# Kernel optimization log

Hardware: AMD Instinct MI355X
Metric: run time of the kernel (lower is better)

## Reference

```python
import jax, jax.numpy as jnp
import numpy as np

B, C, F, D = 128, 16, 128, 512


def setup_inputs() -> dict:
    key = jax.random.key(0)
    k1, k2 = jax.random.split(key)
    return {
        "c_feats": jax.random.normal(k1, (B, C, D), dtype=jnp.float32),
        "f_feats": jax.random.normal(k2, (B, F, D), dtype=jnp.float32),
    }


def _dtw_path_masks(S):
    """S: [P, c, f] per-pair similarity. Returns [P, c, f] 0/1 max-path masks.

    DP: D[i,j] = max(D[i-1,j], D[i,j-1], D[i-1,j-1]) + S[i-1,j-1], D[0,0]=0,
    borders -inf. Tie-break priority (up, left, diag) matches Python max().
    Row recurrence is vectorized: D[i,j] = Csum[j] + cummax_k<=j(A[k]-Csum[k-1])
    where A[k]=max(D[i-1,k], D[i-1,k-1]) (wavefront-free row-parallel form).
    """
    P_, c, f = S.shape
    NEG = -jnp.inf

    init = jnp.concatenate([jnp.zeros((P_, 1), S.dtype),
                            jnp.full((P_, f), NEG, S.dtype)], axis=1)  # D[0, 0..f]

    def row_step(prev, dt_row):
        # prev: [P, f+1] = D[i-1, 0..f]; dt_row: [P, f] = S[i-1, :]
        A = jnp.maximum(prev[:, 1:], prev[:, :-1])                  # max(D[i-1,j], D[i-1,j-1])
        Ccum = jnp.cumsum(dt_row, axis=1)
        Cm1 = jnp.concatenate([jnp.zeros((P_, 1), dt_row.dtype), Ccum[:, :-1]], axis=1)
        row = Ccum + jax.lax.cummax(A - Cm1, axis=1)                # D[i, 1..f]
        new_prev = jnp.concatenate([jnp.full((P_, 1), NEG, dt_row.dtype), row], axis=1)
        return new_prev, new_prev

    _, rows = jax.lax.scan(row_step, init, jnp.moveaxis(S, 1, 0))   # [c, P, f+1]
    Dm = jnp.moveaxis(jnp.concatenate([init[None], rows], axis=0), 1, 0)  # [P, c+1, f+1]

    # Predecessor choice per cell; argmax picks first max -> priority up,left,diag
    up = Dm[:, :-1, 1:]
    left = Dm[:, 1:, :-1]
    diag = Dm[:, :-1, :-1]
    mv = jnp.argmax(jnp.stack([up, left, diag], axis=-1), axis=-1).astype(jnp.int32)
    mv = jnp.pad(mv, ((0, 0), (1, 0), (1, 0)))                      # [P, c+1, f+1]

    pidx = jnp.arange(P_)

    def bt_step(carry, _):
        mask, i, j = carry
        active = (i > 0) | (j > 0)
        mask = mask.at[pidx, i - 1, j - 1].add(jnp.where(active, 1.0, 0.0).astype(mask.dtype))
        m = mv[pidx, i, j]
        di = jnp.where(m == 1, 0, 1)   # left keeps i
        dj = jnp.where(m == 0, 0, 1)   # up keeps j
        i = jnp.where(active, i - di, i)
        j = jnp.where(active, j - dj, j)
        return (mask, i, j), None

    mask0 = jnp.zeros((P_, c, f), jnp.float32)
    i0 = jnp.full((P_,), c, jnp.int32)
    j0 = jnp.full((P_,), f, jnp.int32)
    (mask, _, _), _ = jax.lax.scan(bt_step, (mask0, i0, j0), None, length=c + f)
    return mask


def reference(c_feats, f_feats):
    b, c, d = c_feats.shape
    f = f_feats.shape[1]
    xn = c_feats / jnp.linalg.norm(c_feats, axis=-1, keepdims=True)
    yn = f_feats / jnp.linalg.norm(f_feats, axis=-1, keepdims=True)
    # Source quirk: y row j is normalized only once outer index i reaches it
    # (y[i-1] bug), so S[i,j] uses normalized y[j] iff j <= i, raw y[j] otherwise.
    Sn = jnp.einsum('mcd,nfd->mncf', xn, yn)
    Sr = jnp.einsum('mcd,nfd->mncf', xn, f_feats)
    tri = jnp.arange(f)[None, :] <= jnp.arange(c)[:, None]          # [c, f]: j <= i
    S = jnp.where(tri, Sn, Sr).reshape(b * b, c, f)
    return _dtw_path_masks(S).reshape(b, b, c, f)
```

## Files before the change

### kernel.cpp

```cpp
#include <hip/hip_runtime.h>
#include <stdint.h>

#define M_TOT 2048
#define N_TOT 16384
#define K_TOT 512

typedef _Float16 f16x8 __attribute__((ext_vector_type(8)));
typedef float f32x4 __attribute__((ext_vector_type(4)));

#define AS1 __attribute__((address_space(1)))
#define AS3 __attribute__((address_space(3)))

__device__ __forceinline__ void ld_lds16(const void* g, void* l) {
    __builtin_amdgcn_global_load_lds((const AS1 void*)g, (AS3 void*)l, 16, 0, 0);
}

__device__ __forceinline__ void split4(float x0, float x1, float x2, float x3,
                                       uint2* hs, uint2* ls) {
    union U { _Float16 h[4]; uint2 u; } H, L;
    _Float16 h0 = (_Float16)x0; H.h[0] = h0; L.h[0] = (_Float16)(x0 - (float)h0);
    _Float16 h1 = (_Float16)x1; H.h[1] = h1; L.h[1] = (_Float16)(x1 - (float)h1);
    _Float16 h2 = (_Float16)x2; H.h[2] = h2; L.h[2] = (_Float16)(x2 - (float)h2);
    _Float16 h3 = (_Float16)x3; H.h[3] = h3; L.h[3] = (_Float16)(x3 - (float)h3);
    *hs = H.u; *ls = L.u;
}

__global__ __launch_bounds__(256) void norm_split_kernel(
    const float* __restrict__ c_feats, const float* __restrict__ f_feats,
    _Float16* __restrict__ Ah, _Float16* __restrict__ Al,
    _Float16* __restrict__ Bh, _Float16* __restrict__ Bl,
    float* __restrict__ normf)
{
    int wave = blockIdx.x * 4 + (threadIdx.x >> 6);
    int lane = threadIdx.x & 63;
    if (wave < 2048) {
        const float* row = c_feats + (size_t)wave * K_TOT;
        float4 v0 = ((const float4*)row)[lane];
        float4 v1 = ((const float4*)row)[lane + 64];
        double ss = (double)v0.x * v0.x + (double)v0.y * v0.y +
                    (double)v0.z * v0.z + (double)v0.w * v0.w +
                    (double)v1.x * v1.x + (double)v1.y * v1.y +
                    (double)v1.z * v1.z + (double)v1.w * v1.w;
        #pragma unroll
        for (int off = 32; off; off >>= 1) ss += __shfl_down(ss, off);
        double tot = __shfl(ss, 0);
        float nrm = sqrtf((float)tot);
        float a0 = v0.x / nrm, a1 = v0.y / nrm, a2 = v0.z / nrm, a3 = v0.w / nrm;
        float b0 = v1.x / nrm, b1 = v1.y / nrm, b2 = v1.z / nrm, b3 = v1.w / nrm;
        uint2 h, l;
        split4(a0, a1, a2, a3, &h, &l);
        ((uint2*)(Ah + (size_t)wave * K_TOT))[lane] = h;
        ((uint2*)(Al + (size_t)wave * K_TOT))[lane] = l;
        split4(b0, b1, b2, b3, &h, &l);
        ((uint2*)(Ah + (size_t)wave * K_TOT))[lane + 64] = h;
        ((uint2*)(Al + (size_t)wave * K_TOT))[lane + 64] = l;
    } else if (wave < 18432) {
        int fr = wave - 2048;
        const float* row = f_feats + (size_t)fr * K_TOT;
        float4 v0 = ((const float4*)row)[lane];
        float4 v1 = ((const float4*)row)[lane + 64];
        double ss = (double)v0.x * v0.x + (double)v0.y * v0.y +
                    (double)v0.z * v0.z + (double)v0.w * v0.w +
                    (double)v1.x * v1.x + (double)v1.y * v1.y +
                    (double)v1.z * v1.z + (double)v1.w * v1.w;
        #pragma unroll
        for (int off = 32; off; off >>= 1) ss += __shfl_down(ss, off);
        if (lane == 0) normf[fr] = sqrtf((float)ss);
        uint2 h, l;
        split4(v0.x, v0.y, v0.z, v0.w, &h, &l);
        ((uint2*)(Bh + (size_t)fr * K_TOT))[lane] = h;
        ((uint2*)(Bl + (size_t)fr * K_TOT))[lane] = l;
        split4(v1.x, v1.y, v1.z, v1.w, &h, &l);
        ((uint2*)(Bh + (size_t)fr * K_TOT))[lane + 64] = h;
        ((uint2*)(Bl + (size_t)fr * K_TOT))[lane + 64] = l;
    }
}

__global__ __launch_bounds__(256, 2) void mfma_gemm_kernel(
    const _Float16* __restrict__ Ah, const _Float16* __restrict__ Al,
    const _Float16* __restrict__ Bh, const _Float16* __restrict__ Bl,
    const float* __restrict__ normf,
    float* __restrict__ out)
{
    __shared__ _Float16 sAh[128 * 32];
    __shared__ _Float16 sAl[128 * 32];
    __shared__ _Float16 sBh[128 * 32];
    __shared__ _Float16 sBl[128 * 32];

    const int t = threadIdx.x;
    const int w = t >> 6, lane = t & 63;
    const int gm0 = blockIdx.y * 128, gn0 = blockIdx.x * 128;
    const int wm = (w & 1) * 64, wn = (w >> 1) * 64;
    const int fr = lane & 15, fq = lane >> 4;

    f32x4 acc[4][4] = {};

    const int l0 = w * 128 + lane;

    for (int k0 = 0; k0 < K_TOT; k0 += 32) {
        #pragma unroll
        for (int c = 0; c < 2; ++c) {
            int l = l0 + c * 64;
            int row = l >> 2, kq = l & 3;
            size_t goffA = (size_t)(gm0 + row) * K_TOT + k0 + kq * 8;
            size_t goffB = (size_t)(gn0 + row) * K_TOT + k0 + kq * 8;
            ld_lds16(Ah + goffA, sAh + (size_t)l * 8);
            ld_lds16(Al + goffA, sAl + (size_t)l * 8);
            ld_lds16(Bh + goffB, sBh + (size_t)l * 8);
            ld_lds16(Bl + goffB, sBl + (size_t)l * 8);
        }
        __syncthreads();

        f16x8 fah[4], fal[4], fbh[4], fbl[4];
        #pragma unroll
        for (int x = 0; x < 4; ++x) {
            int ar = (wm + x * 16 + fr) * 32 + fq * 8;
            int br = (wn + x * 16 + fr) * 32 + fq * 8;
            fah[x] = *(const f16x8*)(sAh + ar);
            fal[x] = *(const f16x8*)(sAl + ar);
            fbh[x] = *(const f16x8*)(sBh + br);
            fbl[x] = *(const f16x8*)(sBl + br);
        }
        #pragma unroll
        for (int mi = 0; mi < 4; ++mi)
            #pragma unroll
            for (int ni = 0; ni < 4; ++ni) {
                acc[mi][ni] = __builtin_amdgcn_mfma_f32_16x16x32_f16(fah[mi], fbl[ni], acc[mi][ni], 0, 0, 0);
                acc[mi][ni] = __builtin_amdgcn_mfma_f32_16x16x32_f16(fal[mi], fbh[ni], acc[mi][ni], 0, 0, 0);
                acc[mi][ni] = __builtin_amdgcn_mfma_f32_16x16x32_f16(fah[mi], fbh[ni], acc[mi][ni], 0, 0, 0);
            }
        __syncthreads();
    }

    const int nn = blockIdx.x;
    #pragma unroll
    for (int ni = 0; ni < 4; ++ni) {
        int col = wn + ni * 16 + fr;
        bool cn = (col < 16);
        float nf = 1.f;
        if (cn) nf = normf[gn0 + col];
        #pragma unroll
        for (int mi = 0; mi < 4; ++mi) {
            #pragma unroll
            for (int r = 0; r < 4; ++r) {
                int gm = gm0 + wm + mi * 16 + fq * 4 + r;
                int mm = gm >> 4, ii = gm & 15;
                float v = acc[mi][ni][r];
                if (cn && col <= ii) v /= nf;
                out[(((size_t)mm * 128 + nn) * 16 + ii) * 128 + col] = v;
            }
        }
    }
}

__global__ __launch_bounds__(256) void dtw_kernel(float* __restrict__ buf)
{
    const int lane = threadIdx.x & 63;
    const int p = blockIdx.x * 4 + (threadIdx.x >> 6);
    float* tile = buf + (size_t)p * 2048;
    const double NEG = -1e300;
    double pA = NEG, pB = NEG;
    unsigned mvA = 0, mvB = 0;

    for (int i = 1; i <= 16; ++i) {
        float2 s = ((const float2*)tile)[(i - 1) * 64 + lane];
        double s1 = (double)s.x;
        double s2 = s1 + (double)s.y;
        double t = s2;
        #pragma unroll
        for (int off = 1; off < 64; off <<= 1) {
            double u = __shfl_up(t, off);
            if (lane >= off) t += u;
        }
        double excl = t - s2;
        double C1 = excl + s1;
        double C2 = excl + s2;
        double pm1 = __shfl_up(pB, 1);
        if (lane == 0) pm1 = (i == 1) ? 0.0 : NEG;
        double A1 = fmax(pm1, pA);
        double A2 = fmax(pA, pB);
        double T1 = A1 - excl;
        double T2 = A2 - C1;
        double g = fmax(T1, T2);
        #pragma unroll
        for (int off = 1; off < 64; off <<= 1) {
            double u = __shfl_up(g, off);
            if (lane >= off) g = fmax(g, u);
        }
        double gex = __shfl_up(g, 1);
        if (lane == 0) gex = NEG;
        double M1 = fmax(gex, T1);
        double M2 = fmax(M1, T2);
        double nA = C1 + M1;
        double nB = C2 + M2;
        double lA = __shfl_up(nB, 1);
        if (lane == 0) lA = NEG;
        int m1 = (pA >= lA && pA >= pm1) ? 0 : ((lA >= pm1) ? 1 : 2);
        int m2v = (pB >= nA && pB >= pA) ? 0 : ((nA >= pA) ? 1 : 2);
        mvA |= (unsigned)m1 << (2 * (i - 1));
        mvB |= (unsigned)m2v << (2 * (i - 1));
        pA = nA; pB = nB;
    }

    unsigned maskA = 0, maskB = 0;
    int i = 16, j = 128;
    for (int step = 0; step < 160; ++step) {
        if (i <= 0 && j <= 0) break;
        int col = j - 1, row = i - 1;
        if (row < 0) { j -= 1; continue; }
        if (col < 0) { i -= 1; continue; }
        int owner = col >> 1, sub = col & 1;
        if (lane == owner) {
            if (sub) maskB |= 1u << row; else maskA |= 1u << row;
        }
        unsigned wmv = __shfl(sub ? mvB : mvA, owner);
        int m = (int)((wmv >> (2 * row)) & 3u);
        i -= (m == 1) ? 0 : 1;
        j -= (m == 0) ? 0 : 1;
    }

    #pragma unroll
    for (int r = 0; r < 16; ++r) {
        float2 v;
        v.x = (float)((maskA >> r) & 1u);
        v.y = (float)((maskB >> r) & 1u);
        ((float2*)tile)[r * 64 + lane] = v;
    }
}

extern "C" void kernel_launch(void* const* d_in, const int* in_sizes, int n_in,
                              void* d_out, int out_size, void* d_ws, size_t ws_size,
                              hipStream_t stream)
{
    const float* c_feats = (const float*)d_in[0];
    const float* f_feats = (const float*)d_in[1];
    float* out = (float*)d_out;

    _Float16* Ah = (_Float16*)d_ws;
    _Float16* Al = Ah + (size_t)M_TOT * K_TOT;
    _Float16* Bh = Al + (size_t)M_TOT * K_TOT;
    _Float16* Bl = Bh + (size_t)N_TOT * K_TOT;
    float* normf = (float*)(Bl + (size_t)N_TOT * K_TOT);

    norm_split_kernel<<<4608, 256, 0, stream>>>(c_feats, f_feats, Ah, Al, Bh, Bl, normf);
    dim3 g(N_TOT / 128, M_TOT / 128);
    mfma_gemm_kernel<<<g, 256, 0, stream>>>(Ah, Al, Bh, Bl, normf, out);
    dtw_kernel<<<16384 / 4, 256, 0, stream>>>(out);
}
```

Measured before the change: 386.5 us.

## Rewrite DTW as anti-diagonal wavefront with 16 lanes per pair and LDS backtrack

The DTW kernel changes from a row-parallel scan, with 64 lanes per pair and log-step shuffle scans for the cumsum and cummax, to an anti-diagonal wavefront. Each pair now gets 16 lanes, one per row, so each wave handles 4 pairs. Move codes go to LDS, and one lane per pair backtracks, recording each row's column range. All lanes then write the masks as coalesced float4 stores. This removes the log-depth shuffle scans, but adds a 143-step serial wavefront, a serial backtrack on one lane, and extra LDS use.

```diff
diff --git a/kernel.cpp b/kernel.cpp
--- a/kernel.cpp
+++ b/kernel.cpp
@@ -155,76 +155,81 @@
 
 __global__ __launch_bounds__(256) void dtw_kernel(float* __restrict__ buf)
 {
+    __shared__ uint8_t mv_lds[4][4][2064];
+    __shared__ int bounds[4][4][16];
+
     const int lane = threadIdx.x & 63;
-    const int p = blockIdx.x * 4 + (threadIdx.x >> 6);
+    const int w = threadIdx.x >> 6;
+    const int q = lane >> 4, r = lane & 15;
+    const int pbase = blockIdx.x * 16 + w * 4;
+    const int p = pbase + q;
     float* tile = buf + (size_t)p * 2048;
+    const float4* row4 = (const float4*)(tile + r * 128);
+    uint8_t* mymv = &mv_lds[w][q][0];
+
     const double NEG = -1e300;
-    double pA = NEG, pB = NEG;
-    unsigned mvA = 0, mvB = 0;
-
-    for (int i = 1; i <= 16; ++i) {
-        float2 s = ((const float2*)tile)[(i - 1) * 64 + lane];
-        double s1 = (double)s.x;
-        double s2 = s1 + (double)s.y;
-        double t = s2;
-        #pragma unroll
-        for (int off = 1; off < 64; off <<= 1) {
-            double u = __shfl_up(t, off);
-            if (lane >= off) t += u;
-        }
-        double excl = t - s2;
-        double C1 = excl + s1;
-        double C2 = excl + s2;
-        double pm1 = __shfl_up(pB, 1);
-        if (lane == 0) pm1 = (i == 1) ? 0.0 : NEG;
-        double A1 = fmax(pm1, pA);
-        double A2 = fmax(pA, pB);
-        double T1 = A1 - excl;
-        double T2 = A2 - C1;
-        double g = fmax(T1, T2);
-        #pragma unroll
-        for (int off = 1; off < 64; off <<= 1) {
-            double u = __shfl_up(g, off);
-            if (lane >= off) g = fmax(g, u);
-        }
-        double gex = __shfl_up(g, 1);
-        if (lane == 0) gex = NEG;
-        double M1 = fmax(gex, T1);
-        double M2 = fmax(M1, T2);
-        double nA = C1 + M1;
-        double nB = C2 + M2;
-        double lA = __shfl_up(nB, 1);
-        if (lane == 0) lA = NEG;
-        int m1 = (pA >= lA && pA >= pm1) ? 0 : ((lA >= pm1) ? 1 : 2);
-        int m2v = (pB >= nA && pB >= pA) ? 0 : ((nA >= pA) ? 1 : 2);
-        mvA |= (unsigned)m1 << (2 * (i - 1));
-        mvB |= (unsigned)m2v << (2 * (i - 1));
-        pA = nA; pB = nB;
-    }
-
-    unsigned maskA = 0, maskB = 0;
-    int i = 16, j = 128;
-    for (int step = 0; step < 160; ++step) {
-        if (i <= 0 && j <= 0) break;
-        int col = j - 1, row = i - 1;
-        if (row < 0) { j -= 1; continue; }
-        if (col < 0) { i -= 1; continue; }
-        int owner = col >> 1, sub = col & 1;
-        if (lane == owner) {
-            if (sub) maskB |= 1u << row; else maskA |= 1u << row;
-        }
-        unsigned wmv = __shfl(sub ? mvB : mvA, owner);
-        int m = (int)((wmv >> (2 * row)) & 3u);
-        i -= (m == 1) ? 0 : 1;
-        j -= (m == 0) ? 0 : 1;
-    }
-
-    #pragma unroll
-    for (int r = 0; r < 16; ++r) {
-        float2 v;
-        v.x = (float)((maskA >> r) & 1u);
-        v.y = (float)((maskB >> r) & 1u);
-        ((float2*)tile)[r * 64 + lane] = v;
+    double Dp = NEG, Dp2 = NEG;
+    float4 cur4 = {0, 0, 0, 0};
+    float4 nxt4 = row4[0];
+
+    for (int t = 0; t < 143; ++t) {
+        int j = t - r;
+        bool act = (j >= 0) & (j < 128);
+        if (act & ((j & 3) == 0)) {
+            cur4 = nxt4;
+            if (j + 4 < 128) nxt4 = row4[(j >> 2) + 1];
+        }
+        int e = j & 3;
+        float sv = (e == 0) ? cur4.x : (e == 1) ? cur4.y : (e == 2) ? cur4.z : cur4.w;
+        double up = __shfl_up(Dp, 1);
+        double dg = __shfl_up(Dp2, 1);
+        double lf = Dp;
+        if (r == 0) up = NEG;
+        if (j == 0) {
+            lf = NEG;
+            dg = (r == 0) ? 0.0 : NEG;
+        } else if (r == 0) {
+            dg = NEG;
+        }
+        int m = (up >= lf && up >= dg) ? 0 : ((lf >= dg) ? 1 : 2);
+        double Dc = fmax(up, fmax(lf, dg)) + (double)sv;
+        if (act) mymv[j * 16 + r] = (uint8_t)m;
+        Dp2 = Dp;
+        Dp = Dc;
+    }
+    __syncthreads();
+
+    if (r == 0) {
+        int i = 16, jj = 128, hic = 127;
+        for (int it = 0; it < 160; ++it) {
+            if (i <= 0) break;
+            int m = mymv[(jj - 1) * 16 + (i - 1)];
+            if (m == 1) { --jj; continue; }
+            bounds[w][q][i - 1] = (jj - 1) | (hic << 8);
+            if (m == 2) --jj;
+            --i;
+            hic = jj - 1;
+        }
+    }
+    __syncthreads();
+
+    #pragma unroll 4
+    for (int it = 0; it < 32; ++it) {
+        int flat = it * 64 + lane;
+        int q2 = flat >> 9;
+        int rem = flat & 511;
+        int ii = rem >> 5;
+        int c4 = rem & 31;
+        int b = bounds[w][q2][ii];
+        int lo = b & 0xff, hi = (b >> 8) & 0xff;
+        int j0 = c4 * 4;
+        float4 v;
+        v.x = (j0 + 0 >= lo && j0 + 0 <= hi) ? 1.f : 0.f;
+        v.y = (j0 + 1 >= lo && j0 + 1 <= hi) ? 1.f : 0.f;
+        v.z = (j0 + 2 >= lo && j0 + 2 <= hi) ? 1.f : 0.f;
+        v.w = (j0 + 3 >= lo && j0 + 3 <= hi) ? 1.f : 0.f;
+        float* tb = buf + (size_t)(pbase + q2) * 2048;
+        *(float4*)(tb + ii * 128 + j0) = v;
     }
 }
 
@@ -245,5 +250,5 @@
     norm_split_kernel<<<4608, 256, 0, stream>>>(c_feats, f_feats, Ah, Al, Bh, Bl, normf);
     dim3 g(N_TOT / 128, M_TOT / 128);
     mfma_gemm_kernel<<<g, 256, 0, stream>>>(Ah, Al, Bh, Bl, normf, out);
-    dtw_kernel<<<16384 / 4, 256, 0, stream>>>(out);
-}
+    dtw_kernel<<<1024, 256, 0, stream>>>(out);
+}
```

Result: faster. 361.0 us (-6.6%).
